# Performance work log

Measured on AMD Instinct MI355X. Metric: run time of the kernel, lower is better.

The kernel has to match this reference:

```python
import jax, jax.numpy as jnp
import numpy as np
from jax import lax

EPS = 1e-5
T, N, E = 10, 10000, 320000
C_IN, C_HID, C_OUT = 16, 32, 16


def _stgcn_layer(x, edge_index, edge_weight, tw, tb, gw, gb, gamma, beta):
    # x: [T, N, Cin] -> temporal conv over T per node
    xc = jnp.transpose(x, (1, 2, 0))  # [N, Cin, T]
    y = lax.conv_general_dilated(xc, tw, window_strides=(1,), padding=((1, 1),),
                                 dimension_numbers=("NCH", "OIH", "NCH"))
    y = y + tb[None, :, None]
    y = jnp.clip(y, -10.0, 10.0)
    # InstanceNorm1d (affine, biased var over time axis)
    mu = jnp.mean(y, axis=-1, keepdims=True)
    var = jnp.mean((y - mu) ** 2, axis=-1, keepdims=True)
    y = (y - mu) * lax.rsqrt(var + EPS) * gamma[None, :, None] + beta[None, :, None]
    y = jax.nn.relu(y)
    h = jnp.transpose(y, (0, 2, 1))  # [N, T, C]

    n = h.shape[0]
    # GCNConv normalization (identical at every timestep -> computed once)
    ewn = jax.nn.softmax(edge_weight)  # softmax over all E edges
    loop = jnp.arange(n, dtype=edge_index.dtype)
    row = jnp.concatenate([edge_index[0], loop])  # sources (+self loops)
    col = jnp.concatenate([edge_index[1], loop])  # destinations
    w = jnp.concatenate([ewn, jnp.ones((n,), dtype=ewn.dtype)])
    deg = jax.ops.segment_sum(w, col, num_segments=n)
    dinv = jnp.where(deg > 0, lax.rsqrt(jnp.maximum(deg, EPS * 0 + 1e-30)), 0.0)
    norm = dinv[row] * w * dinv[col]  # [E+N]

    hw = jnp.einsum("ntc,cd->ntd", h, gw)  # [N, T, C]
    msg = hw[row] * norm[:, None, None]     # [E+N, T, C] gather
    agg = jax.ops.segment_sum(msg, col, num_segments=n) + gb  # scatter-add
    out = jnp.clip(jax.nn.relu(agg), -10.0, 10.0)
    return jnp.transpose(out, (1, 0, 2))  # [T, N, C]


def setup_inputs() -> dict:
    key = jax.random.key(0)
    ks = jax.random.split(key, 16)
    inp = {
        "x": jax.random.normal(ks[0], (T, N, C_IN), dtype=jnp.float32),
        "edge_index": jax.random.randint(ks[1], (2, E), 0, N, dtype=jnp.int32),
        "edge_weight": jax.random.uniform(ks[2], (E,), dtype=jnp.float32),
        # layer 1 (in -> hid)
        "l1_tw": jax.random.normal(ks[3], (C_HID, C_IN, 3), dtype=jnp.float32) * 0.02,
        "l1_tb": jnp.zeros((C_HID,), dtype=jnp.float32),
        "l1_gw": jax.random.normal(ks[4], (C_HID, C_HID), dtype=jnp.float32) * 0.1,
        "l1_gb": jnp.zeros((C_HID,), dtype=jnp.float32),
        "l1_gamma": jnp.ones((C_HID,), dtype=jnp.float32),
        "l1_beta": jnp.zeros((C_HID,), dtype=jnp.float32),
        # layer 2 (hid -> hid)
        "l2_tw": jax.random.normal(ks[5], (C_HID, C_HID, 3), dtype=jnp.float32) * 0.02,
        "l2_tb": jnp.zeros((C_HID,), dtype=jnp.float32),
        "l2_gw": jax.random.normal(ks[6], (C_HID, C_HID), dtype=jnp.float32) * 0.1,
        "l2_gb": jnp.zeros((C_HID,), dtype=jnp.float32),
        "l2_gamma": jnp.ones((C_HID,), dtype=jnp.float32),
        "l2_beta": jnp.zeros((C_HID,), dtype=jnp.float32),
        # output linear
        "out_w": jax.random.normal(ks[7], (C_HID, C_OUT), dtype=jnp.float32) * 0.1,
        "out_b": jnp.zeros((C_OUT,), dtype=jnp.float32),
    }
    return inp


def reference(x, edge_index, edge_weight,
              l1_tw, l1_tb, l1_gw, l1_gb, l1_gamma, l1_beta,
              l2_tw, l2_tb, l2_gw, l2_gb, l2_gamma, l2_beta,
              out_w, out_b):
    h = _stgcn_layer(x, edge_index, edge_weight, l1_tw, l1_tb, l1_gw, l1_gb, l1_gamma, l1_beta)
    h = _stgcn_layer(h, edge_index, edge_weight, l2_tw, l2_tb, l2_gw, l2_gb, l2_gamma, l2_beta)
    # per-timestep linear then mean over time == mean then linear, done faithfully
    outs = jnp.einsum("tnc,cd->tnd", h, out_w) + out_b
    return jnp.mean(outs, axis=0)  # [N, C_OUT]
```

## Files before the change

kernel.cpp:

```cpp
#include <hip/hip_runtime.h>
#include <hip/hip_bf16.h>
#include <string.h>


typedef __hip_bfloat16 bf16;

#define TSTEPS 10
#define TPAD 12
#define CHID 32
#define ROWELE (TSTEPS * CHID)
#define ROWW4 40

__device__ __forceinline__ float b2f(bf16 v) { return __bfloat162float(v); }
__device__ __forceinline__ float ldf(const void* p, long i, int bf) {
    return bf ? __bfloat162float(((const bf16*)p)[i]) : ((const float*)p)[i];
}
__device__ __forceinline__ int detect_bf(const unsigned* gbits) {
    return (gbits[0] != 0x3F800000u) ? 1 : 0;
}
__device__ __forceinline__ float bflo(unsigned u) { return __uint_as_float(u << 16); }
__device__ __forceinline__ float bfhi(unsigned u) { return __uint_as_float(u & 0xFFFF0000u); }
__device__ __forceinline__ unsigned pack2bf(float a, float b) {
    bf16 x = __float2bfloat16(a), y = __float2bfloat16(b);
    unsigned short ux, uy;
    memcpy(&ux, &x, 2); memcpy(&uy, &y, 2);
    return (unsigned)ux | ((unsigned)uy << 16);
}
__device__ __forceinline__ void accum8(float* f, uint4 u, float w) {
    f[0] += w * bflo(u.x); f[1] += w * bfhi(u.x);
    f[2] += w * bflo(u.y); f[3] += w * bfhi(u.y);
    f[4] += w * bflo(u.z); f[5] += w * bfhi(u.z);
    f[6] += w * bflo(u.w); f[7] += w * bfhi(u.w);
}


__global__ __launch_bounds__(256) void edge_pass_kernel(
    const void* __restrict__ ew, const unsigned* __restrict__ gbits,
    const int* __restrict__ ei,
    float* __restrict__ ewn, float* __restrict__ degx, int* __restrict__ cnt,
    float* sumexp, int E) {
    int bf = detect_bf(gbits);
    int i = blockIdx.x * 256 + threadIdx.x;
    float e = 0.0f;
    if (i < E) {
        float w = ldf(ew, i, bf);
        e = __expf(w);
        ewn[i] = e;
        int c = ei[E + i];
        atomicAdd(&degx[c], e);
        atomicAdd(&cnt[c], 1);
    }
    float v = e;
    for (int o = 32; o > 0; o >>= 1) v += __shfl_down(v, o);
    __shared__ float s[4];
    int lane = threadIdx.x & 63, wv = threadIdx.x >> 6;
    if (lane == 0) s[wv] = v;
    __syncthreads();
    if (threadIdx.x == 0) atomicAdd(sumexp, s[0] + s[1] + s[2] + s[3]);
}

__global__ __launch_bounds__(1024) void scan_kernel(const int* __restrict__ cnt,
                                                    const float* __restrict__ degx,
                                                    const float* __restrict__ sumexp,
                                                    float* __restrict__ dinv,
                                                    int* __restrict__ off, int N) {
    __shared__ int s[1024];
    int tid = threadIdx.x;
    float invS = 1.0f / (*sumexp);
    for (int i = tid; i < N; i += 1024) dinv[i] = rsqrtf(1.0f + degx[i] * invS);
    int chunk = (N + 1023) / 1024;
    int b0 = tid * chunk;
    int p = 0;
    for (int k = 0; k < chunk; k++) { int i = b0 + k; if (i < N) p += cnt[i]; }
    s[tid] = p;
    __syncthreads();
    for (int d = 1; d < 1024; d <<= 1) {
        int v = (tid >= d) ? s[tid - d] : 0;
        __syncthreads();
        s[tid] += v;
        __syncthreads();
    }
    int base = s[tid] - p;
    for (int k = 0; k < chunk; k++) {
        int i = b0 + k;
        if (i < N) {
            off[i] = base;
            base += cnt[i];
            if (i == N - 1) off[N] = base;
        }
    }
}

__global__ __launch_bounds__(256) void fill_kernel(const int* __restrict__ ei,
                                                   const float* __restrict__ ewn,
                                                   const float* __restrict__ dinv,
                                                   const float* __restrict__ sumexp,
                                                   const int* __restrict__ off,
                                                   int* __restrict__ cursor,
                                                   int* __restrict__ csr_src,
                                                   float* __restrict__ csr_w, int E) {
    int i = blockIdx.x * 256 + threadIdx.x;
    if (i >= E) return;
    float invS = 1.0f / (*sumexp);
    int r = ei[i], c = ei[E + i];
    int p = atomicAdd(&cursor[c], 1);
    int idx = off[c] + p;
    csr_src[idx] = r;
    csr_w[idx] = dinv[r] * (ewn[i] * invS) * dinv[c];
}


template <int CIN, int LAYOUT>
__global__ __launch_bounds__(256) void conv_kernel(
    const void* __restrict__ in_, const unsigned* __restrict__ gbits,
    const void* __restrict__ tw, const void* __restrict__ tb,
    const void* __restrict__ gamma, const void* __restrict__ beta,
    const void* __restrict__ gw,
    bf16* __restrict__ hw, int N) {
    constexpr int CO = CHID;
    __shared__ __align__(16) float s_in[8 * CIN * TPAD];
    __shared__ __align__(16) float s_h[8 * CO * TPAD];
    __shared__ float s_tw[3 * CIN * CO];
    __shared__ float s_gw[CO * CO];
    __shared__ float s_tb[CO], s_ga[CO], s_be[CO];

    int bfw = detect_bf(gbits);
    int tid = threadIdx.x;
    for (int i = tid; i < CO * CIN * 3; i += 256) {
        int o = i / (CIN * 3);
        int rem = i % (CIN * 3);
        int ci = rem / 3, k = rem % 3;
        s_tw[(k * CIN + ci) * CO + o] = ldf(tw, i, bfw);
    }
    for (int i = tid; i < CO * CO; i += 256) s_gw[i] = ldf(gw, i, bfw);
    if (tid < CO) {
        s_tb[tid] = ldf(tb, tid, bfw);
        s_ga[tid] = ldf(gamma, tid, bfw);
        s_be[tid] = ldf(beta, tid, bfw);
    }

    int nb = blockIdx.x * 8;

    if (LAYOUT == 0) {
        constexpr int CP = CIN / 2;
        for (int i2 = tid; i2 < 8 * TSTEPS * CP; i2 += 256) {
            int cp = i2 % CP;
            int t = (i2 / CP) % TSTEPS;
            int nl = i2 / (CP * TSTEPS);
            int n = nb + nl;
            float v0 = 0.0f, v1 = 0.0f;
            if (n < N) {
                long idx = (long)t * ((long)N * CIN) + (long)n * CIN + 2 * cp;
                if (bfw) {
                    unsigned u = ((const unsigned*)in_)[idx >> 1];
                    v0 = bflo(u); v1 = bfhi(u);
                } else {
                    float2 f = ((const float2*)in_)[idx >> 1];
                    v0 = f.x; v1 = f.y;
                }
            }
            int b = nl * (CIN * TPAD) + (2 * cp) * TPAD + t;
            s_in[b] = v0;
            s_in[b + TPAD] = v1;
        }
    } else {
        for (int i2 = tid; i2 < 8 * CIN * 5; i2 += 256) {
            int tp = i2 % 5;
            int ci = (i2 / 5) % CIN;
            int nl = i2 / (5 * CIN);
            int n = nb + nl;
            float v0 = 0.0f, v1 = 0.0f;
            if (n < N) {
                long idx = (long)n * (CIN * TSTEPS) + ci * TSTEPS + 2 * tp;
                unsigned u = ((const unsigned*)in_)[idx >> 1];
                v0 = bflo(u); v1 = bfhi(u);
            }
            int b = nl * (CIN * TPAD) + ci * TPAD + 2 * tp;
            s_in[b] = v0;
            s_in[b + 1] = v1;
        }
    }
    __syncthreads();

    int nl = tid >> 5, o = tid & 31;
    int n = nb + nl;
    const float* xrow = &s_in[nl * CIN * TPAD];

    float acc[TSTEPS];
    float tbv = s_tb[o];
#pragma unroll
    for (int t = 0; t < TSTEPS; t++) acc[t] = tbv;

    for (int ci = 0; ci < CIN; ci++) {
        const float4* xp = (const float4*)&xrow[ci * TPAD];
        float4 A = xp[0], B = xp[1], C = xp[2];
        float xr[TSTEPS] = {A.x, A.y, A.z, A.w, B.x, B.y, B.z, B.w, C.x, C.y};
        float w0 = s_tw[(0 * CIN + ci) * CO + o];
        float w1 = s_tw[(1 * CIN + ci) * CO + o];
        float w2 = s_tw[(2 * CIN + ci) * CO + o];
        acc[0] += xr[0] * w1 + xr[1] * w2;
#pragma unroll
        for (int t = 1; t < TSTEPS - 1; t++)
            acc[t] += xr[t - 1] * w0 + xr[t] * w1 + xr[t + 1] * w2;
        acc[TSTEPS - 1] += xr[TSTEPS - 2] * w0 + xr[TSTEPS - 1] * w1;
    }

#pragma unroll
    for (int t = 0; t < TSTEPS; t++) acc[t] = fminf(fmaxf(acc[t], -10.0f), 10.0f);
    float mu = 0.0f;
#pragma unroll
    for (int t = 0; t < TSTEPS; t++) mu += acc[t];
    mu *= 0.1f;
    float var = 0.0f;
#pragma unroll
    for (int t = 0; t < TSTEPS; t++) { float d = acc[t] - mu; var += d * d; }
    var *= 0.1f;
    float sc = s_ga[o] * rsqrtf(var + 1e-5f);
    float be = s_be[o];
    float h[TSTEPS];
#pragma unroll
    for (int t = 0; t < TSTEPS; t++) h[t] = fmaxf((acc[t] - mu) * sc + be, 0.0f);

    float4* hp = (float4*)&s_h[nl * CO * TPAD + o * TPAD];
    hp[0] = make_float4(h[0], h[1], h[2], h[3]);
    hp[1] = make_float4(h[4], h[5], h[6], h[7]);
    hp[2] = make_float4(h[8], h[9], 0.0f, 0.0f);
    __syncthreads();

    float acc2[TSTEPS];
#pragma unroll
    for (int t = 0; t < TSTEPS; t++) acc2[t] = 0.0f;
    const float* hrow = &s_h[nl * CO * TPAD];
    for (int c = 0; c < CO; c++) {
        const float4* cp4 = (const float4*)&hrow[c * TPAD];
        float4 A = cp4[0], B = cp4[1], C = cp4[2];
        float g = s_gw[c * CO + o];
        acc2[0] += A.x * g; acc2[1] += A.y * g; acc2[2] += A.z * g; acc2[3] += A.w * g;
        acc2[4] += B.x * g; acc2[5] += B.y * g; acc2[6] += B.z * g; acc2[7] += B.w * g;
        acc2[8] += C.x * g; acc2[9] += C.y * g;
    }
    if (n < N) {
        unsigned* hwp = (unsigned*)hw;
        long base = (long)n * (ROWELE / 2) + o * (TSTEPS / 2);
#pragma unroll
        for (int j = 0; j < 5; j++)
            hwp[base + j] = pack2bf(acc2[2 * j], acc2[2 * j + 1]);
    }
}


template <bool FINAL>
__global__ __launch_bounds__(320) void agg_kernel_t(
    const uint4* __restrict__ hw4, const int* __restrict__ off,
    const int* __restrict__ csr_src, const float* __restrict__ csr_w,
    const float* __restrict__ dinv, const void* __restrict__ gb,
    const void* __restrict__ ow, const void* __restrict__ ob,
    const unsigned* __restrict__ gbits,
    void* __restrict__ out, int N) {
    __shared__ int s_src[ROWELE];
    __shared__ float s_w[ROWELE];
    __shared__ float s_part[8 * ROWW4 * 9];
    __shared__ float s_hbar[CHID];
    __shared__ float s_ow[CHID * 16];
    __shared__ float s_ob[16];

    int bf = detect_bf(gbits);
    int n = blockIdx.x;
    int tid = threadIdx.x;
    int g = tid % ROWW4;
    int eo = tid / ROWW4;

    if (FINAL) {
        for (int i = tid; i < CHID * 16; i += ROWELE) s_ow[i] = ldf(ow, i, bf);
        if (tid < 16) s_ob[tid] = ldf(ob, tid, bf);
    }

    float facc[8];
#pragma unroll
    for (int j = 0; j < 8; j++) facc[j] = 0.0f;

    float dn = dinv[n];
    if (eo == 0) {
        uint4 u = hw4[n * ROWW4 + g];
        accum8(facc, u, dn * dn);
    }

    int beg = off[n], end = off[n + 1];
    for (int base = beg; base < end; base += ROWELE) {
        int m = min(ROWELE, end - base);
        if (tid < m) { s_src[tid] = csr_src[base + tid]; s_w[tid] = csr_w[base + tid]; }
        __syncthreads();
        int kmax = (m + 7) >> 3;
        int k = 0;
        for (; k + 2 <= kmax; k += 2) {
            int j0 = (k << 3) + eo, j1 = j0 + 8;
            int c0 = min(j0, m - 1), c1 = min(j1, m - 1);
            float w0 = (j0 < m) ? s_w[c0] : 0.0f;
            float w1 = (j1 < m) ? s_w[c1] : 0.0f;
            int r0 = s_src[c0], r1 = s_src[c1];
            uint4 u0 = hw4[r0 * ROWW4 + g];
            uint4 u1 = hw4[r1 * ROWW4 + g];
            accum8(facc, u0, w0);
            accum8(facc, u1, w1);
        }
        if (k < kmax) {
            int j0 = (k << 3) + eo;
            int c0 = min(j0, m - 1);
            float w0 = (j0 < m) ? s_w[c0] : 0.0f;
            int r0 = s_src[c0];
            uint4 u0 = hw4[r0 * ROWW4 + g];
            accum8(facc, u0, w0);
        }
        __syncthreads();
    }

    {
        float* rowp = &s_part[(eo * ROWW4 + g) * 9];
#pragma unroll
        for (int j = 0; j < 8; j++) rowp[j] = facc[j];
    }
    __syncthreads();
    int gg = tid >> 3, jj = tid & 7;
    float v = 0.0f;
#pragma unroll
    for (int s = 0; s < 8; s++) v += s_part[(s * ROWW4 + gg) * 9 + jj];
    int c = tid / TSTEPS;
    v += ldf(gb, c, bf);
    v = fminf(fmaxf(v, 0.0f), 10.0f);

    if (!FINAL) {
        ((bf16*)out)[(long)n * ROWELE + tid] = __float2bfloat16(v);
    } else {
        __syncthreads();
        s_part[tid] = v;
        __syncthreads();
        if (tid < CHID) {
            float s = 0.0f;
#pragma unroll
            for (int t = 0; t < TSTEPS; t++) s += s_part[tid * TSTEPS + t];
            s_hbar[tid] = s * 0.1f;
        }
        __syncthreads();
        if (tid < 16) {
            float a = s_ob[tid];
#pragma unroll
            for (int cc = 0; cc < CHID; cc++) a += s_hbar[cc] * s_ow[cc * 16 + tid];
            long oi = (long)n * 16 + tid;
            if (bf) ((bf16*)out)[oi] = __float2bfloat16(a);
            else    ((float*)out)[oi] = a;
        }
    }
}


extern "C" void kernel_launch(void* const* d_in, const int* in_sizes, int n_in,
                              void* d_out, int out_size, void* d_ws, size_t ws_size,
                              hipStream_t stream) {
    (void)n_in; (void)out_size; (void)ws_size;

    const void* x     = d_in[0];
    const int*  ei    = (const int*)d_in[1];
    const void* ew    = d_in[2];
    const void* l1_tw = d_in[3];
    const void* l1_tb = d_in[4];
    const void* l1_gw = d_in[5];
    const void* l1_gb = d_in[6];
    const unsigned* gbits = (const unsigned*)d_in[7];
    const void* l1_ga = d_in[7];
    const void* l1_be = d_in[8];
    const void* l2_tw = d_in[9];
    const void* l2_tb = d_in[10];
    const void* l2_gw = d_in[11];
    const void* l2_gb = d_in[12];
    const void* l2_ga = d_in[13];
    const void* l2_be = d_in[14];
    const void* out_w = d_in[15];
    const void* out_b = d_in[16];

    const int N = in_sizes[0] / (TSTEPS * 16);
    const int E = in_sizes[1] / 2;

    char* p = (char*)d_ws;
    auto alloc = [&](size_t bytes) -> char* {
        char* r = p;
        p += (bytes + 255) & ~(size_t)255;
        return r;
    };
    char* zbase   = p;
    float* sumexp = (float*)alloc(256);
    float* degx   = (float*)alloc((size_t)N * 4);
    int*   cnt    = (int*)alloc((size_t)N * 4);
    int*   cursor = (int*)alloc((size_t)N * 4);
    size_t zbytes = (size_t)(p - zbase);
    float* ewn     = (float*)alloc((size_t)E * 4);
    float* dinv    = (float*)alloc((size_t)N * 4);
    int*   offA    = (int*)alloc((size_t)(N + 1) * 4);
    int*   csr_src = (int*)alloc((size_t)E * 4);
    float* csr_w   = (float*)alloc((size_t)E * 4);
    bf16*  bufA    = (bf16*)alloc((size_t)N * ROWELE * 2);
    bf16*  bufB    = (bf16*)alloc((size_t)N * ROWELE * 2);

    int gE = (E + 255) / 256;
    int gConv = (N + 7) / 8;

    hipMemsetAsync(zbase, 0, zbytes, stream);
    hipLaunchKernelGGL(edge_pass_kernel, dim3(gE), dim3(256), 0, stream,
                       ew, gbits, ei, ewn, degx, cnt, sumexp, E);
    hipLaunchKernelGGL(scan_kernel, dim3(1), dim3(1024), 0, stream,
                       cnt, degx, sumexp, dinv, offA, N);
    hipLaunchKernelGGL(fill_kernel, dim3(gE), dim3(256), 0, stream,
                       ei, ewn, dinv, sumexp, offA, cursor, csr_src, csr_w, E);

    hipLaunchKernelGGL((conv_kernel<16, 0>), dim3(gConv), dim3(256), 0, stream,
                       x, gbits, l1_tw, l1_tb, l1_ga, l1_be, l1_gw, bufA, N);
    hipLaunchKernelGGL((agg_kernel_t<false>), dim3(N), dim3(ROWELE), 0, stream,
                       (const uint4*)bufA, offA, csr_src, csr_w, dinv, l1_gb,
                       nullptr, nullptr, gbits, (void*)bufB, N);
    hipLaunchKernelGGL((conv_kernel<32, 1>), dim3(gConv), dim3(256), 0, stream,
                       (const void*)bufB, gbits, l2_tw, l2_tb, l2_ga, l2_be, l2_gw, bufA, N);
    hipLaunchKernelGGL((agg_kernel_t<true>), dim3(N), dim3(ROWELE), 0, stream,
                       (const uint4*)bufA, offA, csr_src, csr_w, dinv, l2_gb,
                       out_w, out_b, gbits, d_out, N);
}
```

Measured before the change: 287.4 us.

## Vectorize edge kernels, interleave CSR src/weight, pack conv weights as bf16

The edge-pass and fill kernels now handle four edges per thread with vector loads, launching a quarter as many blocks. CSR source indices and weights are interleaved into a single int2 array, so the aggregation kernel does one load per edge instead of two. The conv kernel stores its temporal and graph weights in shared memory as packed bf16, reads bias, gamma and beta straight into registers, and gets a launch-bounds occupancy hint. This trims memory traffic and shared-memory footprint, but rounding the conv weights to bf16 adds precision loss even on fp32 inputs.

Measured after the change: 340.9 us. 1.19x slower.

```diff
diff --git a/kernel.cpp b/kernel.cpp
--- a/kernel.cpp
+++ b/kernel.cpp
@@ -26,6 +26,11 @@
     memcpy(&ux, &x, 2); memcpy(&uy, &y, 2);
     return (unsigned)ux | ((unsigned)uy << 16);
 }
+__device__ __forceinline__ unsigned short bfbits(float a) {
+    bf16 x = __float2bfloat16(a);
+    unsigned short u; memcpy(&u, &x, 2);
+    return u;
+}
 __device__ __forceinline__ void accum8(float* f, uint4 u, float w) {
     f[0] += w * bflo(u.x); f[1] += w * bfhi(u.x);
     f[2] += w * bflo(u.y); f[3] += w * bfhi(u.y);
@@ -40,17 +45,40 @@
     float* __restrict__ ewn, float* __restrict__ degx, int* __restrict__ cnt,
     float* sumexp, int E) {
     int bf = detect_bf(gbits);
-    int i = blockIdx.x * 256 + threadIdx.x;
-    float e = 0.0f;
-    if (i < E) {
-        float w = ldf(ew, i, bf);
-        e = __expf(w);
-        ewn[i] = e;
-        int c = ei[E + i];
-        atomicAdd(&degx[c], e);
-        atomicAdd(&cnt[c], 1);
-    }
-    float v = e;
+    int i0 = (blockIdx.x * 256 + threadIdx.x) * 4;
+    float e0 = 0.0f, e1 = 0.0f, e2 = 0.0f, e3 = 0.0f;
+    if ((E & 3) == 0 && i0 + 3 < E) {
+        float w0, w1, w2, w3;
+        if (bf) {
+            uint2 u = ((const uint2*)ew)[i0 >> 2];
+            w0 = bflo(u.x); w1 = bfhi(u.x); w2 = bflo(u.y); w3 = bfhi(u.y);
+        } else {
+            float4 f = ((const float4*)ew)[i0 >> 2];
+            w0 = f.x; w1 = f.y; w2 = f.z; w3 = f.w;
+        }
+        e0 = __expf(w0); e1 = __expf(w1); e2 = __expf(w2); e3 = __expf(w3);
+        int4 c4 = *(const int4*)&ei[E + i0];
+        atomicAdd(&degx[c4.x], e0); atomicAdd(&cnt[c4.x], 1);
+        atomicAdd(&degx[c4.y], e1); atomicAdd(&cnt[c4.y], 1);
+        atomicAdd(&degx[c4.z], e2); atomicAdd(&cnt[c4.z], 1);
+        atomicAdd(&degx[c4.w], e3); atomicAdd(&cnt[c4.w], 1);
+        *(float4*)&ewn[i0] = make_float4(e0, e1, e2, e3);
+    } else {
+        float es[4] = {0, 0, 0, 0};
+        for (int j = 0; j < 4; j++) {
+            int i = i0 + j;
+            if (i < E) {
+                float e = __expf(ldf(ew, i, bf));
+                es[j] = e;
+                ewn[i] = e;
+                int c = ei[E + i];
+                atomicAdd(&degx[c], e);
+                atomicAdd(&cnt[c], 1);
+            }
+        }
+        e0 = es[0]; e1 = es[1]; e2 = es[2]; e3 = es[3];
+    }
+    float v = (e0 + e1) + (e2 + e3);
     for (int o = 32; o > 0; o >>= 1) v += __shfl_down(v, o);
     __shared__ float s[4];
     int lane = threadIdx.x & 63, wv = threadIdx.x >> 6;
@@ -91,27 +119,46 @@
     }
 }
 
+
 __global__ __launch_bounds__(256) void fill_kernel(const int* __restrict__ ei,
                                                    const float* __restrict__ ewn,
                                                    const float* __restrict__ dinv,
                                                    const float* __restrict__ sumexp,
                                                    const int* __restrict__ off,
                                                    int* __restrict__ cursor,
-                                                   int* __restrict__ csr_src,
-                                                   float* __restrict__ csr_w, int E) {
-    int i = blockIdx.x * 256 + threadIdx.x;
-    if (i >= E) return;
+                                                   int2* __restrict__ csr, int E) {
+    int i0 = (blockIdx.x * 256 + threadIdx.x) * 4;
+    if (i0 >= E) return;
     float invS = 1.0f / (*sumexp);
-    int r = ei[i], c = ei[E + i];
-    int p = atomicAdd(&cursor[c], 1);
-    int idx = off[c] + p;
-    csr_src[idx] = r;
-    csr_w[idx] = dinv[r] * (ewn[i] * invS) * dinv[c];
+    if ((E & 3) == 0 && i0 + 3 < E) {
+        int4 r4 = *(const int4*)&ei[i0];
+        int4 c4 = *(const int4*)&ei[E + i0];
+        float4 e4 = *(const float4*)&ewn[i0];
+        int rr[4] = {r4.x, r4.y, r4.z, r4.w};
+        int cc[4] = {c4.x, c4.y, c4.z, c4.w};
+        float ee[4] = {e4.x, e4.y, e4.z, e4.w};
+#pragma unroll
+        for (int j = 0; j < 4; j++) {
+            int r = rr[j], c = cc[j];
+            int p = atomicAdd(&cursor[c], 1);
+            float w = dinv[r] * (ee[j] * invS) * dinv[c];
+            csr[off[c] + p] = make_int2(r, __float_as_int(w));
+        }
+    } else {
+        for (int j = 0; j < 4; j++) {
+            int i = i0 + j;
+            if (i >= E) break;
+            int r = ei[i], c = ei[E + i];
+            int p = atomicAdd(&cursor[c], 1);
+            float w = dinv[r] * (ewn[i] * invS) * dinv[c];
+            csr[off[c] + p] = make_int2(r, __float_as_int(w));
+        }
+    }
 }
 
 
 template <int CIN, int LAYOUT>
-__global__ __launch_bounds__(256) void conv_kernel(
+__global__ __launch_bounds__(256, 5) void conv_kernel(
     const void* __restrict__ in_, const unsigned* __restrict__ gbits,
     const void* __restrict__ tw, const void* __restrict__ tb,
     const void* __restrict__ gamma, const void* __restrict__ beta,
@@ -120,23 +167,31 @@
     constexpr int CO = CHID;
     __shared__ __align__(16) float s_in[8 * CIN * TPAD];
     __shared__ __align__(16) float s_h[8 * CO * TPAD];
-    __shared__ float s_tw[3 * CIN * CO];
-    __shared__ float s_gw[CO * CO];
-    __shared__ float s_tb[CO], s_ga[CO], s_be[CO];
+    __shared__ __align__(16) unsigned s_tw01[CIN * CO];
+    __shared__ __align__(16) unsigned short s_tw2[CIN * CO];
+    __shared__ __align__(16) unsigned s_gwp[(CO / 2) * CO];
 
     int bfw = detect_bf(gbits);
     int tid = threadIdx.x;
-    for (int i = tid; i < CO * CIN * 3; i += 256) {
-        int o = i / (CIN * 3);
-        int rem = i % (CIN * 3);
-        int ci = rem / 3, k = rem % 3;
-        s_tw[(k * CIN + ci) * CO + o] = ldf(tw, i, bfw);
-    }
-    for (int i = tid; i < CO * CO; i += 256) s_gw[i] = ldf(gw, i, bfw);
-    if (tid < CO) {
-        s_tb[tid] = ldf(tb, tid, bfw);
-        s_ga[tid] = ldf(gamma, tid, bfw);
-        s_be[tid] = ldf(beta, tid, bfw);
+    int nl = tid >> 5, o = tid & 31;
+
+    float tbv = ldf(tb, o, bfw);
+    float gav = ldf(gamma, o, bfw);
+    float bev = ldf(beta, o, bfw);
+
+    for (int i = tid; i < CIN * CO; i += 256) {
+        int ci = i / CO, oo = i % CO;
+        long base = ((long)oo * CIN + ci) * 3;
+        float w0 = ldf(tw, base, bfw);
+        float w1 = ldf(tw, base + 1, bfw);
+        float w2 = ldf(tw, base + 2, bfw);
+        s_tw01[ci * CO + oo] = pack2bf(w0, w1);
+        s_tw2[ci * CO + oo] = bfbits(w2);
+    }
+    for (int i = tid; i < (CO / 2) * CO; i += 256) {
+        int cp = i / CO, oo = i % CO;
+        s_gwp[i] = pack2bf(ldf(gw, (long)(2 * cp) * CO + oo, bfw),
+                           ldf(gw, (long)(2 * cp + 1) * CO + oo, bfw));
     }
 
     int nb = blockIdx.x * 8;
@@ -146,8 +201,8 @@
         for (int i2 = tid; i2 < 8 * TSTEPS * CP; i2 += 256) {
             int cp = i2 % CP;
             int t = (i2 / CP) % TSTEPS;
-            int nl = i2 / (CP * TSTEPS);
-            int n = nb + nl;
+            int nn = i2 / (CP * TSTEPS);
+            int n = nb + nn;
             float v0 = 0.0f, v1 = 0.0f;
             if (n < N) {
                 long idx = (long)t * ((long)N * CIN) + (long)n * CIN + 2 * cp;
@@ -159,7 +214,7 @@
                     v0 = f.x; v1 = f.y;
                 }
             }
-            int b = nl * (CIN * TPAD) + (2 * cp) * TPAD + t;
+            int b = nn * (CIN * TPAD) + (2 * cp) * TPAD + t;
             s_in[b] = v0;
             s_in[b + TPAD] = v1;
         }
@@ -167,27 +222,25 @@
         for (int i2 = tid; i2 < 8 * CIN * 5; i2 += 256) {
             int tp = i2 % 5;
             int ci = (i2 / 5) % CIN;
-            int nl = i2 / (5 * CIN);
-            int n = nb + nl;
+            int nn = i2 / (5 * CIN);
+            int n = nb + nn;
             float v0 = 0.0f, v1 = 0.0f;
             if (n < N) {
                 long idx = (long)n * (CIN * TSTEPS) + ci * TSTEPS + 2 * tp;
                 unsigned u = ((const unsigned*)in_)[idx >> 1];
                 v0 = bflo(u); v1 = bfhi(u);
             }
-            int b = nl * (CIN * TPAD) + ci * TPAD + 2 * tp;
+            int b = nn * (CIN * TPAD) + ci * TPAD + 2 * tp;
             s_in[b] = v0;
             s_in[b + 1] = v1;
         }
     }
     __syncthreads();
 
-    int nl = tid >> 5, o = tid & 31;
     int n = nb + nl;
     const float* xrow = &s_in[nl * CIN * TPAD];
 
     float acc[TSTEPS];
-    float tbv = s_tb[o];
 #pragma unroll
     for (int t = 0; t < TSTEPS; t++) acc[t] = tbv;
 
@@ -195,9 +248,9 @@
         const float4* xp = (const float4*)&xrow[ci * TPAD];
         float4 A = xp[0], B = xp[1], C = xp[2];
         float xr[TSTEPS] = {A.x, A.y, A.z, A.w, B.x, B.y, B.z, B.w, C.x, C.y};
-        float w0 = s_tw[(0 * CIN + ci) * CO + o];
-        float w1 = s_tw[(1 * CIN + ci) * CO + o];
-        float w2 = s_tw[(2 * CIN + ci) * CO + o];
+        unsigned w01 = s_tw01[ci * CO + o];
+        float w0 = bflo(w01), w1 = bfhi(w01);
+        float w2 = __uint_as_float(((unsigned)s_tw2[ci * CO + o]) << 16);
         acc[0] += xr[0] * w1 + xr[1] * w2;
 #pragma unroll
         for (int t = 1; t < TSTEPS - 1; t++)
@@ -215,11 +268,10 @@
 #pragma unroll
     for (int t = 0; t < TSTEPS; t++) { float d = acc[t] - mu; var += d * d; }
     var *= 0.1f;
-    float sc = s_ga[o] * rsqrtf(var + 1e-5f);
-    float be = s_be[o];
+    float sc = gav * rsqrtf(var + 1e-5f);
     float h[TSTEPS];
 #pragma unroll
-    for (int t = 0; t < TSTEPS; t++) h[t] = fmaxf((acc[t] - mu) * sc + be, 0.0f);
+    for (int t = 0; t < TSTEPS; t++) h[t] = fmaxf((acc[t] - mu) * sc + bev, 0.0f);
 
     float4* hp = (float4*)&s_h[nl * CO * TPAD + o * TPAD];
     hp[0] = make_float4(h[0], h[1], h[2], h[3]);
@@ -231,13 +283,23 @@
 #pragma unroll
     for (int t = 0; t < TSTEPS; t++) acc2[t] = 0.0f;
     const float* hrow = &s_h[nl * CO * TPAD];
-    for (int c = 0; c < CO; c++) {
-        const float4* cp4 = (const float4*)&hrow[c * TPAD];
-        float4 A = cp4[0], B = cp4[1], C = cp4[2];
-        float g = s_gw[c * CO + o];
-        acc2[0] += A.x * g; acc2[1] += A.y * g; acc2[2] += A.z * g; acc2[3] += A.w * g;
-        acc2[4] += B.x * g; acc2[5] += B.y * g; acc2[6] += B.z * g; acc2[7] += B.w * g;
-        acc2[8] += C.x * g; acc2[9] += C.y * g;
+    for (int cp = 0; cp < CO / 2; cp++) {
+        unsigned g2 = s_gwp[cp * CO + o];
+        float g0 = bflo(g2), g1 = bfhi(g2);
+        const float4* r0 = (const float4*)&hrow[(2 * cp) * TPAD];
+        const float4* r1 = (const float4*)&hrow[(2 * cp + 1) * TPAD];
+        float4 A0 = r0[0], B0 = r0[1], C0 = r0[2];
+        float4 A1 = r1[0], B1 = r1[1], C1 = r1[2];
+        acc2[0] += A0.x * g0 + A1.x * g1;
+        acc2[1] += A0.y * g0 + A1.y * g1;
+        acc2[2] += A0.z * g0 + A1.z * g1;
+        acc2[3] += A0.w * g0 + A1.w * g1;
+        acc2[4] += B0.x * g0 + B1.x * g1;
+        acc2[5] += B0.y * g0 + B1.y * g1;
+        acc2[6] += B0.z * g0 + B1.z * g1;
+        acc2[7] += B0.w * g0 + B1.w * g1;
+        acc2[8] += C0.x * g0 + C1.x * g1;
+        acc2[9] += C0.y * g0 + C1.y * g1;
     }
     if (n < N) {
         unsigned* hwp = (unsigned*)hw;
@@ -252,13 +314,12 @@
 template <bool FINAL>
 __global__ __launch_bounds__(320) void agg_kernel_t(
     const uint4* __restrict__ hw4, const int* __restrict__ off,
-    const int* __restrict__ csr_src, const float* __restrict__ csr_w,
+    const int2* __restrict__ csr,
     const float* __restrict__ dinv, const void* __restrict__ gb,
     const void* __restrict__ ow, const void* __restrict__ ob,
     const unsigned* __restrict__ gbits,
     void* __restrict__ out, int N) {
-    __shared__ int s_src[ROWELE];
-    __shared__ float s_w[ROWELE];
+    __shared__ int2 s_sw[ROWELE];
     __shared__ float s_part[8 * ROWW4 * 9];
     __shared__ float s_hbar[CHID];
     __shared__ float s_ow[CHID * 16];
@@ -288,27 +349,27 @@
     int beg = off[n], end = off[n + 1];
     for (int base = beg; base < end; base += ROWELE) {
         int m = min(ROWELE, end - base);
-        if (tid < m) { s_src[tid] = csr_src[base + tid]; s_w[tid] = csr_w[base + tid]; }
+        if (tid < m) s_sw[tid] = csr[base + tid];
         __syncthreads();
         int kmax = (m + 7) >> 3;
         int k = 0;
         for (; k + 2 <= kmax; k += 2) {
             int j0 = (k << 3) + eo, j1 = j0 + 8;
             int c0 = min(j0, m - 1), c1 = min(j1, m - 1);
-            float w0 = (j0 < m) ? s_w[c0] : 0.0f;
-            float w1 = (j1 < m) ? s_w[c1] : 0.0f;
-            int r0 = s_src[c0], r1 = s_src[c1];
-            uint4 u0 = hw4[r0 * ROWW4 + g];
-            uint4 u1 = hw4[r1 * ROWW4 + g];
+            int2 e0 = s_sw[c0], e1 = s_sw[c1];
+            float w0 = (j0 < m) ? __int_as_float(e0.y) : 0.0f;
+            float w1 = (j1 < m) ? __int_as_float(e1.y) : 0.0f;
+            uint4 u0 = hw4[e0.x * ROWW4 + g];
+            uint4 u1 = hw4[e1.x * ROWW4 + g];
             accum8(facc, u0, w0);
             accum8(facc, u1, w1);
         }
         if (k < kmax) {
             int j0 = (k << 3) + eo;
             int c0 = min(j0, m - 1);
-            float w0 = (j0 < m) ? s_w[c0] : 0.0f;
-            int r0 = s_src[c0];
-            uint4 u0 = hw4[r0 * ROWW4 + g];
+            int2 e0 = s_sw[c0];
+            float w0 = (j0 < m) ? __int_as_float(e0.y) : 0.0f;
+            uint4 u0 = hw4[e0.x * ROWW4 + g];
             accum8(facc, u0, w0);
         }
         __syncthreads();
@@ -395,30 +456,29 @@
     float* ewn     = (float*)alloc((size_t)E * 4);
     float* dinv    = (float*)alloc((size_t)N * 4);
     int*   offA    = (int*)alloc((size_t)(N + 1) * 4);
-    int*   csr_src = (int*)alloc((size_t)E * 4);
-    float* csr_w   = (float*)alloc((size_t)E * 4);
+    int2*  csr     = (int2*)alloc((size_t)E * 8);
     bf16*  bufA    = (bf16*)alloc((size_t)N * ROWELE * 2);
     bf16*  bufB    = (bf16*)alloc((size_t)N * ROWELE * 2);
 
-    int gE = (E + 255) / 256;
+    int gE4 = (E + 1023) / 1024;
     int gConv = (N + 7) / 8;
 
     hipMemsetAsync(zbase, 0, zbytes, stream);
-    hipLaunchKernelGGL(edge_pass_kernel, dim3(gE), dim3(256), 0, stream,
+    hipLaunchKernelGGL(edge_pass_kernel, dim3(gE4), dim3(256), 0, stream,
                        ew, gbits, ei, ewn, degx, cnt, sumexp, E);
     hipLaunchKernelGGL(scan_kernel, dim3(1), dim3(1024), 0, stream,
                        cnt, degx, sumexp, dinv, offA, N);
-    hipLaunchKernelGGL(fill_kernel, dim3(gE), dim3(256), 0, stream,
-                       ei, ewn, dinv, sumexp, offA, cursor, csr_src, csr_w, E);
+    hipLaunchKernelGGL(fill_kernel, dim3(gE4), dim3(256), 0, stream,
+                       ei, ewn, dinv, sumexp, offA, cursor, csr, E);
 
     hipLaunchKernelGGL((conv_kernel<16, 0>), dim3(gConv), dim3(256), 0, stream,
                        x, gbits, l1_tw, l1_tb, l1_ga, l1_be, l1_gw, bufA, N);
     hipLaunchKernelGGL((agg_kernel_t<false>), dim3(N), dim3(ROWELE), 0, stream,
-                       (const uint4*)bufA, offA, csr_src, csr_w, dinv, l1_gb,
+                       (const uint4*)bufA, offA, csr, dinv, l1_gb,
                        nullptr, nullptr, gbits, (void*)bufB, N);
     hipLaunchKernelGGL((conv_kernel<32, 1>), dim3(gConv), dim3(256), 0, stream,
                        (const void*)bufB, gbits, l2_tw, l2_tb, l2_ga, l2_be, l2_gw, bufA, N);
     hipLaunchKernelGGL((agg_kernel_t<true>), dim3(N), dim3(ROWELE), 0, stream,
-                       (const uint4*)bufA, offA, csr_src, csr_w, dinv, l2_gb,
+                       (const uint4*)bufA, offA, csr, dinv, l2_gb,
                        out_w, out_b, gbits, d_out, N);
 }
```
